# Kernel tuning notes

Hardware: AMD Instinct MI355X
Metric: run time of the kernel (lower is better)

The kernel has to match this reference:

```python
import jax, jax.numpy as jnp
import numpy as np

# irreps: 16x0e + 8x1o ; sh: 1x0e + 1x1o
M0, M1 = 16, 8
N_NODES, N_EDGES, N_BASIS = 10000, 160000, 8
DIM = M0 + 3 * M1                      # 40
NW = M0*M0 + M0*M1 + M1*M1 + M1*M0     # 576 per-edge TP weights
LOG2 = 0.6931471805599453


def _split(x):
    return x[:, :M0], x[:, M0:].reshape(-1, M1, 3)


def _merge(xs, xv):
    return jnp.concatenate([xs, xv.reshape(xv.shape[0], -1)], axis=1)


def _lin(x, Ws, Wv):
    # e3nn o3.Linear: per-irrep channel mixing, 1/sqrt(fan_in) path norm
    xs, xv = _split(x)
    return _merge(xs @ Ws / np.sqrt(M0),
                  jnp.einsum('nui,uv->nvi', xv, Wv) / np.sqrt(M1))


def _ssp(x):  # ShiftedSoftPlus
    return jax.nn.softplus(x) - LOG2


def setup_inputs() -> dict:
    key = jax.random.key(0)
    k = jax.random.split(key, 14)
    return {
        'x': jax.random.normal(k[0], (N_NODES, DIM), jnp.float32),
        'edge_radial': jax.random.uniform(k[1], (N_EDGES, N_BASIS), dtype=jnp.float32),
        'edge_sh': jax.random.normal(k[2], (N_EDGES, 4), jnp.float32),
        'edge_src': jax.random.randint(k[3], (N_EDGES,), 0, N_NODES),
        'edge_dst': jax.random.randint(k[4], (N_EDGES,), 0, N_NODES),
        'n_nodes': N_NODES,
        'W1s': jax.random.normal(k[5], (M0, M0), jnp.float32),
        'W1v': jax.random.normal(k[6], (M1, M1), jnp.float32),
        'Wfc': jax.random.normal(k[7], (N_BASIS, NW), jnp.float32),
        'W2s': jax.random.normal(k[8], (M0, M0), jnp.float32),
        'W2v': jax.random.normal(k[9], (M1, M1), jnp.float32),
        'R00': jax.random.normal(k[10], (M0, M0, M0), jnp.float32),
        'R01': jax.random.normal(k[11], (M0, M1, M1), jnp.float32),
        'R10': jax.random.normal(k[12], (M1, M0, M1), jnp.float32),
        'R11': jax.random.normal(k[13], (M1, M1, M0), jnp.float32),
    }


def reference(x, edge_radial, edge_sh, edge_src, edge_dst, n_nodes,
              W1s, W1v, Wfc, W2s, W2v, R00, R01, R10, R11):
    inv2 = 1.0 / np.sqrt(2.0)

    # linear_1
    h = _lin(x, W1s, W1v)
    hs, hv = _split(h)

    # SO3Convolution: per-edge TP weights from radial net
    sh0, sh1 = edge_sh[:, 0], edge_sh[:, 1:4]
    w = edge_radial @ Wfc / np.sqrt(N_BASIS)  # [E, NW]
    o = 0
    w00 = w[:, o:o + M0*M0].reshape(-1, M0, M0); o += M0*M0  # 0e x 0e -> 0e
    w01 = w[:, o:o + M0*M1].reshape(-1, M0, M1); o += M0*M1  # 0e x 1o -> 1o
    w10 = w[:, o:o + M1*M1].reshape(-1, M1, M1); o += M1*M1  # 1o x 0e -> 1o
    w11 = w[:, o:o + M1*M0].reshape(-1, M1, M0)              # 1o x 1o -> 0e (CG: delta/sqrt(3))

    xs_e, xv_e = hs[edge_src], hv[edge_src]  # gather
    msg_s = (jnp.einsum('eu,e,euw->ew', xs_e, sh0, w00) / np.sqrt(M0)
             + jnp.einsum('eui,ei,euw->ew', xv_e, sh1, w11) / np.sqrt(3.0 * M1)) * inv2
    msg_v = (jnp.einsum('eu,ei,euw->ewi', xs_e, sh1, w01) / np.sqrt(M0)
             + jnp.einsum('eui,e,euw->ewi', xv_e, sh0, w10) / np.sqrt(M1)) * inv2

    deg = np.sqrt(N_EDGES / N_NODES)
    outs = jax.ops.segment_sum(msg_s, edge_dst, num_segments=n_nodes) / deg
    outv = jax.ops.segment_sum(msg_v, edge_dst, num_segments=n_nodes) / deg

    # linear_2
    h = _lin(_merge(outs, outv), W2s, W2v)
    hs, hv = _split(h)

    # NormActivation (normalize=True, ShiftedSoftPlus, eps=1e-8)
    eps = 1e-8
    ns = jnp.sqrt(hs * hs + eps * eps)
    hs = hs / ns * _ssp(ns)
    nv = jnp.sqrt(jnp.sum(hv * hv, -1, keepdims=True) + eps * eps)
    hv = hv / nv * _ssp(nv)
    out = _merge(hs, hv)

    # residual FullyConnectedTensorProduct(x, x)
    xs, xv = _split(x)
    rs = (jnp.einsum('nu,nv,uvw->nw', xs, xs, R00) / M0
          + jnp.einsum('nui,nvi,uvw->nw', xv, xv, R11) / np.sqrt(3.0 * M1 * M1)) * inv2
    rv = (jnp.einsum('nu,nvi,uvw->nwi', xs, xv, R01) / np.sqrt(M0 * M1)
          + jnp.einsum('nui,nv,uvw->nwi', xv, xs, R10) / np.sqrt(M1 * M0)) * inv2

    return out + _merge(rs, rv)
```

## Files before the change

kernel.cpp:

```cpp
#include <hip/hip_runtime.h>
#include <math.h>

constexpr int kM0 = 16, kM1 = 8, kDim = 40, kNW = 576;
constexpr int kNodes = 10000, kEdges = 160000;
constexpr int kCap = 96;
constexpr int kNB = 24;

__device__ __forceinline__ float sspf(float x){
  float ax = fabsf(x);
  return fmaxf(x, 0.f) + log1pf(expf(-ax)) - 0.69314718055994531f;
}

__global__ void __launch_bounds__(256) k_pre(
    const float* __restrict__ x, const float* __restrict__ W1s,
    const float* __restrict__ W1v, const float* __restrict__ Wfc,
    const int* __restrict__ edst,
    float* __restrict__ h, float* __restrict__ WfcT,
    int* __restrict__ cnt, int* __restrict__ posw){
  int t = blockIdx.x*256 + threadIdx.x;
  posw[t] = atomicAdd(&cnt[edst[t]], 1);
  if (t < kNW){
    #pragma unroll
    for (int b=0;b<8;++b) WfcT[t*8+b] = Wfc[b*kNW + t];
  }
  if (t < kNodes){
    const float4* xp4 = (const float4*)(x + (size_t)t*kDim);
    float xx[40];
    #pragma unroll
    for (int i=0;i<10;++i){
      float4 v = xp4[i];
      xx[i*4]=v.x; xx[i*4+1]=v.y; xx[i*4+2]=v.z; xx[i*4+3]=v.w;
    }
    float hh[40];
    #pragma unroll
    for (int v=0; v<kM0; ++v){
      float acc = 0.f;
      #pragma unroll
      for (int u=0; u<kM0; ++u) acc += xx[u]*W1s[u*kM0+v];
      hh[v] = acc*0.25f;
    }
    #pragma unroll
    for (int v=0; v<kM1; ++v){
      float a0=0.f,a1=0.f,a2=0.f;
      #pragma unroll
      for (int u=0; u<kM1; ++u){
        float wv = W1v[u*kM1+v];
        a0 += xx[16+u*3+0]*wv;
        a1 += xx[16+u*3+1]*wv;
        a2 += xx[16+u*3+2]*wv;
      }
      hh[16+v*3+0]=a0*0.35355339059327373f;
      hh[16+v*3+1]=a1*0.35355339059327373f;
      hh[16+v*3+2]=a2*0.35355339059327373f;
    }
    float4* hp4 = (float4*)(h + (size_t)t*kDim);
    #pragma unroll
    for (int i=0;i<10;++i)
      hp4[i] = make_float4(hh[i*4],hh[i*4+1],hh[i*4+2],hh[i*4+3]);
  }
}

__global__ void __launch_bounds__(512) k_edge(
    const float* __restrict__ er, const float* __restrict__ esh,
    const int* __restrict__ esrc, const int* __restrict__ edst,
    const int* __restrict__ posw,
    const float* __restrict__ h, const float* __restrict__ WfcT,
    float* __restrict__ msg){
  __shared__ float sh_h[64][41];
  int t = threadIdx.x;
  int e0 = blockIdx.x*64;
  for (int idx = t; idx < 640; idx += 512){
    int el = idx/10, c4 = idx - el*10;
    int src = esrc[e0 + el];
    const float4 v = *(const float4*)(h + (size_t)src*kDim + c4*4);
    float* d = &sh_h[el][c4*4];
    d[0]=v.x; d[1]=v.y; d[2]=v.z; d[3]=v.w;
  }
  __syncthreads();

  int lane = t & 63;
  int q = __builtin_amdgcn_readfirstlane(t >> 6);
  int e = e0 + lane;
  float4 ra = *(const float4*)(er + (size_t)e*8);
  float4 rb = *(const float4*)(er + (size_t)e*8 + 4);
  const float r0=ra.x,r1=ra.y,r2=ra.z,r3=ra.w,r4=rb.x,r5=rb.y,r6=rb.z,r7=rb.w;
  float4 s4 = *(const float4*)(esh + (size_t)e*4);
  const float* hl = sh_h[lane];
  float* mp = msg + ((size_t)edst[e]*kCap + posw[e])*kDim;

#define DOT8(p) ((p)[0]*r0+(p)[1]*r1+(p)[2]*r2+(p)[3]*r3+(p)[4]*r4+(p)[5]*r5+(p)[6]*r6+(p)[7]*r7)

  const int w0 = q*2;
  float t00a=0.f, t00b=0.f, t11a=0.f, t11b=0.f;
  float t01=0.f, tx=0.f, ty=0.f, tz=0.f;

  #pragma unroll
  for (int u=0;u<16;++u){
    float xu = hl[u];
    const float* p0 = WfcT + (size_t)(u*16 + w0)*8;
    t00a += xu*DOT8(p0);
    t00b += xu*DOT8(p0 + 8);
    const float* p1 = WfcT + (size_t)(256 + u*8 + q)*8;
    t01 += xu*DOT8(p1);
  }
  #pragma unroll
  for (int u=0;u<8;++u){
    float v0=hl[16+u*3], v1=hl[16+u*3+1], v2=hl[16+u*3+2];
    float au = v0*s4.y + v1*s4.z + v2*s4.w;
    const float* p3 = WfcT + (size_t)(448 + u*16 + w0)*8;
    t11a += au*DOT8(p3);
    t11b += au*DOT8(p3 + 8);
    const float* p2 = WfcT + (size_t)(384 + u*8 + q)*8;
    float a = DOT8(p2);
    tx += v0*a; ty += v1*a; tz += v2*a;
  }
#undef DOT8

  constexpr float cs00 = 0.0625f;
  constexpr float cs11 = 0.05103103630798288f;
  constexpr float cv01 = 0.0625f;
  constexpr float cv10 = 0.08838834764831845f;

  *(float2*)(mp + w0) = make_float2(s4.x*t00a*cs00 + t11a*cs11,
                                    s4.x*t00b*cs00 + t11b*cs11);
  float va = t01*cv01, sc0 = s4.x*cv10;
  float* vp = mp + 16 + q*3;
  vp[0] = s4.y*va + tx*sc0;
  vp[1] = s4.z*va + ty*sc0;
  vp[2] = s4.w*va + tz*sc0;
}

__global__ void __launch_bounds__(960) k_node(
    const float* __restrict__ x, const float* __restrict__ msg,
    const int* __restrict__ cnt,
    const float* __restrict__ W2s, const float* __restrict__ W2v,
    const float* __restrict__ R00, const float* __restrict__ R01,
    const float* __restrict__ R10, const float* __restrict__ R11,
    float* __restrict__ out){
  __shared__ float sR00[4096], sR01[1024], sR10[1024], sR11[1024];
  __shared__ float sW2s[256], sW2v[64];
  __shared__ float sx[kNB][40], sa[kNB][40];
  __shared__ float4 sred[kNB][4][10];
  int t = threadIdx.x;
  for (int i=t; i<1024; i+=960) ((float4*)sR00)[i] = ((const float4*)R00)[i];
  if (t < 256){
    ((float4*)sR01)[t] = ((const float4*)R01)[t];
    ((float4*)sR10)[t] = ((const float4*)R10)[t];
    ((float4*)sR11)[t] = ((const float4*)R11)[t];
  }
  if (t >= 256 && t < 320) ((float4*)sW2s)[t-256] = ((const float4*)W2s)[t-256];
  if (t >= 320 && t < 336) ((float4*)sW2v)[t-320] = ((const float4*)W2v)[t-320];
  int nb = blockIdx.x*kNB;
  {
    int ns = t/40; int rem = t - ns*40; int kq = rem/10; int c4 = rem - kq*10;
    int n = nb + ns;
    float4 acc = make_float4(0.f,0.f,0.f,0.f);
    if (n < kNodes){
      int deg = cnt[n];
      const float* bp = msg + (size_t)n*kCap*kDim + c4*4;
      for (int k=kq; k<deg; k+=4){
        const float4 v = *(const float4*)(bp + (size_t)k*kDim);
        acc.x+=v.x; acc.y+=v.y; acc.z+=v.z; acc.w+=v.w;
      }
    }
    sred[ns][kq][c4] = acc;
  }
  __syncthreads();
  if (t < kNB*10){
    int ns = t/10, c4 = t - ns*10, n = nb+ns;
    float4 a0 = sred[ns][0][c4], a1 = sred[ns][1][c4];
    float4 a2 = sred[ns][2][c4], a3 = sred[ns][3][c4];
    sa[ns][c4*4+0] = (a0.x+a1.x+a2.x+a3.x)*0.25f;
    sa[ns][c4*4+1] = (a0.y+a1.y+a2.y+a3.y)*0.25f;
    sa[ns][c4*4+2] = (a0.z+a1.z+a2.z+a3.z)*0.25f;
    sa[ns][c4*4+3] = (a0.w+a1.w+a2.w+a3.w)*0.25f;
    float4 xv = (n < kNodes) ? *(const float4*)(x + (size_t)n*kDim + c4*4)
                             : make_float4(0.f,0.f,0.f,0.f);
    sx[ns][c4*4+0]=xv.x; sx[ns][c4*4+1]=xv.y; sx[ns][c4*4+2]=xv.z; sx[ns][c4*4+3]=xv.w;
  }
  __syncthreads();
  if (t < kNB*16){
    int ns = t>>4, w = t&15, n = nb+ns;
    const float* ap = sa[ns];
    const float* xp = sx[ns];
    float hsum = 0.f;
    #pragma unroll
    for (int u=0;u<16;++u) hsum += ap[u]*sW2s[u*16+w];
    hsum *= 0.25f;
    float nrm = sqrtf(hsum*hsum + 1e-16f);
    float val = hsum/nrm*sspf(nrm);
    float xs[16];
    #pragma unroll
    for (int v=0;v<16;++v) xs[v] = xp[v];
    float r0 = 0.f;
    #pragma unroll
    for (int u=0;u<16;++u){
      float tacc = 0.f;
      #pragma unroll
      for (int v=0;v<16;++v) tacc += xs[v]*sR00[(u*16+v)*16+w];
      r0 += xs[u]*tacc;
    }
    float xv[24];
    #pragma unroll
    for (int c2=0;c2<24;++c2) xv[c2] = xp[16+c2];
    float r1 = 0.f;
    #pragma unroll
    for (int u=0;u<8;++u){
      #pragma unroll
      for (int v=0;v<8;++v){
        float dot = xv[u*3]*xv[v*3] + xv[u*3+1]*xv[v*3+1] + xv[u*3+2]*xv[v*3+2];
        r1 += dot*sR11[(u*8+v)*16+w];
      }
    }
    if (n < kNodes)
      out[(size_t)n*kDim + w] = val + 0.04419417382415922f*r0 + 0.05103103630798288f*r1;
  } else if (t >= kNB*16 && t < kNB*16 + kNB*24) {
    int t2 = t - kNB*16;
    int ns = t2/24, cc = t2 - ns*24, w = cc/3, i = cc - w*3, n = nb+ns;
    const float* ap = sa[ns] + 16;
    const float* xp = sx[ns];
    float h0=0.f,h1=0.f,h2=0.f;
    #pragma unroll
    for (int u=0;u<8;++u){
      float wv = sW2v[u*8+w];
      h0 += ap[u*3+0]*wv; h1 += ap[u*3+1]*wv; h2 += ap[u*3+2]*wv;
    }
    const float sc = 0.35355339059327373f;
    h0*=sc; h1*=sc; h2*=sc;
    float nv = sqrtf(h0*h0+h1*h1+h2*h2 + 1e-16f);
    float hi = (i==0)?h0:((i==1)?h1:h2);
    float val = hi/nv*sspf(nv);
    float xs[16];
    #pragma unroll
    for (int v=0;v<16;++v) xs[v] = xp[v];
    float xvi[8];
    #pragma unroll
    for (int v=0;v<8;++v) xvi[v] = xp[16+v*3+i];
    float racc = 0.f;
    #pragma unroll
    for (int u=0;u<16;++u){
      float tacc=0.f;
      #pragma unroll
      for (int v=0;v<8;++v) tacc += xvi[v]*sR01[(u*8+v)*8+w];
      racc += xs[u]*tacc;
    }
    #pragma unroll
    for (int u=0;u<8;++u){
      float tacc=0.f;
      #pragma unroll
      for (int v=0;v<16;++v) tacc += xs[v]*sR10[(u*16+v)*8+w];
      racc += xvi[u]*tacc;
    }
    if (n < kNodes)
      out[(size_t)n*kDim + 16 + cc] = val + 0.0625f*racc;
  }
}

extern "C" void kernel_launch(void* const* d_in, const int* in_sizes, int n_in,
                              void* d_out, int out_size, void* d_ws, size_t ws_size,
                              hipStream_t stream){
  const float* x   = (const float*)d_in[0];
  const float* er  = (const float*)d_in[1];
  const float* esh = (const float*)d_in[2];
  const int*   esrc= (const int*)d_in[3];
  const int*   edst= (const int*)d_in[4];
  const float* W1s = (const float*)d_in[6];
  const float* W1v = (const float*)d_in[7];
  const float* Wfc = (const float*)d_in[8];
  const float* W2s = (const float*)d_in[9];
  const float* W2v = (const float*)d_in[10];
  const float* R00 = (const float*)d_in[11];
  const float* R01 = (const float*)d_in[12];
  const float* R10 = (const float*)d_in[13];
  const float* R11 = (const float*)d_in[14];
  float* out = (float*)d_out;

  char* wsb = (char*)d_ws;
  float* h    = (float*)wsb;
  float* msg  = h + (size_t)kNodes*kDim;
  float* WfcT = msg + (size_t)kNodes*kCap*kDim;
  int*   cnt  = (int*)(WfcT + (size_t)kNW*8);
  int*   posw = cnt + kNodes;

  hipMemsetAsync(cnt, 0, kNodes*sizeof(int), stream);
  k_pre<<<kEdges/256, 256, 0, stream>>>(x, W1s, W1v, Wfc, edst, h, WfcT, cnt, posw);
  k_edge<<<kEdges/64, 512, 0, stream>>>(er, esh, esrc, edst, posw, h, WfcT, msg);
  k_node<<<(kNodes+kNB-1)/kNB, 960, 0, stream>>>(x, msg, cnt, W2s, W2v, R00, R01, R10, R11, out);
}
```

Measured before the change: 155.1 us.

## Fuse linear_1 and destination slot assignment into edge kernel, drop memset

Moves the per-node linear_1 into the edge kernel: each block gathers raw x rows for its 64 source nodes into shared memory and applies W1s/W1v there, so the intermediate h buffer is no longer written and read. The per-edge atomic slot assignment also moves into the edge kernel, which removes the posw array. The memset of the counters becomes a tiny setup kernel that also transposes Wfc. The cost is that linear_1 is recomputed once per edge instead of once per node (16x redundant), and there is an extra barrier plus more shared memory per block.

```diff
diff --git a/kernel.cpp b/kernel.cpp
--- a/kernel.cpp
+++ b/kernel.cpp
@@ -11,82 +11,75 @@
   return fmaxf(x, 0.f) + log1pf(expf(-ax)) - 0.69314718055994531f;
 }
 
-__global__ void __launch_bounds__(256) k_pre(
-    const float* __restrict__ x, const float* __restrict__ W1s,
-    const float* __restrict__ W1v, const float* __restrict__ Wfc,
-    const int* __restrict__ edst,
-    float* __restrict__ h, float* __restrict__ WfcT,
-    int* __restrict__ cnt, int* __restrict__ posw){
-  int t = blockIdx.x*256 + threadIdx.x;
-  posw[t] = atomicAdd(&cnt[edst[t]], 1);
+__global__ void __launch_bounds__(1024) k_setup(
+    const float* __restrict__ Wfc, float* __restrict__ WfcT, int* __restrict__ cnt){
+  int t = blockIdx.x*1024 + threadIdx.x;
+  if (t < kNodes) cnt[t] = 0;
   if (t < kNW){
     #pragma unroll
     for (int b=0;b<8;++b) WfcT[t*8+b] = Wfc[b*kNW + t];
-  }
-  if (t < kNodes){
-    const float4* xp4 = (const float4*)(x + (size_t)t*kDim);
-    float xx[40];
-    #pragma unroll
-    for (int i=0;i<10;++i){
-      float4 v = xp4[i];
-      xx[i*4]=v.x; xx[i*4+1]=v.y; xx[i*4+2]=v.z; xx[i*4+3]=v.w;
-    }
-    float hh[40];
-    #pragma unroll
-    for (int v=0; v<kM0; ++v){
-      float acc = 0.f;
-      #pragma unroll
-      for (int u=0; u<kM0; ++u) acc += xx[u]*W1s[u*kM0+v];
-      hh[v] = acc*0.25f;
-    }
-    #pragma unroll
-    for (int v=0; v<kM1; ++v){
-      float a0=0.f,a1=0.f,a2=0.f;
-      #pragma unroll
-      for (int u=0; u<kM1; ++u){
-        float wv = W1v[u*kM1+v];
-        a0 += xx[16+u*3+0]*wv;
-        a1 += xx[16+u*3+1]*wv;
-        a2 += xx[16+u*3+2]*wv;
-      }
-      hh[16+v*3+0]=a0*0.35355339059327373f;
-      hh[16+v*3+1]=a1*0.35355339059327373f;
-      hh[16+v*3+2]=a2*0.35355339059327373f;
-    }
-    float4* hp4 = (float4*)(h + (size_t)t*kDim);
-    #pragma unroll
-    for (int i=0;i<10;++i)
-      hp4[i] = make_float4(hh[i*4],hh[i*4+1],hh[i*4+2],hh[i*4+3]);
   }
 }
 
 __global__ void __launch_bounds__(512) k_edge(
     const float* __restrict__ er, const float* __restrict__ esh,
     const int* __restrict__ esrc, const int* __restrict__ edst,
-    const int* __restrict__ posw,
-    const float* __restrict__ h, const float* __restrict__ WfcT,
-    float* __restrict__ msg){
+    const float* __restrict__ x, const float* __restrict__ W1s,
+    const float* __restrict__ W1v, const float* __restrict__ WfcT,
+    float* __restrict__ msg, int* __restrict__ cnt){
+  __shared__ float sh_x[64][41];
   __shared__ float sh_h[64][41];
+  __shared__ int   smp[64];
   int t = threadIdx.x;
+  int lane = t & 63;
+  int q = __builtin_amdgcn_readfirstlane(t >> 6);
   int e0 = blockIdx.x*64;
+
+  int myoff = 0;
+  if (q == 0){
+    int dst = edst[e0 + lane];
+    int pos = atomicAdd(&cnt[dst], 1);
+    myoff = (dst*kCap + pos)*kDim;
+  }
   for (int idx = t; idx < 640; idx += 512){
     int el = idx/10, c4 = idx - el*10;
     int src = esrc[e0 + el];
-    const float4 v = *(const float4*)(h + (size_t)src*kDim + c4*4);
-    float* d = &sh_h[el][c4*4];
+    const float4 v = *(const float4*)(x + (size_t)src*kDim + c4*4);
+    float* d = &sh_x[el][c4*4];
     d[0]=v.x; d[1]=v.y; d[2]=v.z; d[3]=v.w;
   }
-  __syncthreads();
-
-  int lane = t & 63;
-  int q = __builtin_amdgcn_readfirstlane(t >> 6);
+  if (q == 0) smp[lane] = myoff;
+  __syncthreads();
+
+  {
+    #pragma unroll
+    for (int k=0;k<5;++k){
+      const int c = q + 8*k;
+      float o;
+      if (c < 16){
+        float acc=0.f;
+        #pragma unroll
+        for (int u=0;u<16;++u) acc += sh_x[lane][u]*W1s[u*16+c];
+        o = acc*0.25f;
+      } else {
+        int j = c-16; int v = j/3, i = j-3*v;
+        float acc=0.f;
+        #pragma unroll
+        for (int u=0;u<8;++u) acc += sh_x[lane][16+u*3+i]*W1v[u*8+v];
+        o = acc*0.35355339059327373f;
+      }
+      sh_h[lane][c] = o;
+    }
+  }
+  __syncthreads();
+
   int e = e0 + lane;
   float4 ra = *(const float4*)(er + (size_t)e*8);
   float4 rb = *(const float4*)(er + (size_t)e*8 + 4);
   const float r0=ra.x,r1=ra.y,r2=ra.z,r3=ra.w,r4=rb.x,r5=rb.y,r6=rb.z,r7=rb.w;
   float4 s4 = *(const float4*)(esh + (size_t)e*4);
   const float* hl = sh_h[lane];
-  float* mp = msg + ((size_t)edst[e]*kCap + posw[e])*kDim;
+  float* mp = msg + smp[lane];
 
 #define DOT8(p) ((p)[0]*r0+(p)[1]*r1+(p)[2]*r2+(p)[3]*r3+(p)[4]*r4+(p)[5]*r5+(p)[6]*r6+(p)[7]*r7)
 
@@ -214,7 +207,7 @@
     }
     if (n < kNodes)
       out[(size_t)n*kDim + w] = val + 0.04419417382415922f*r0 + 0.05103103630798288f*r1;
-  } else if (t >= kNB*16 && t < kNB*16 + kNB*24) {
+  } else if (t < kNB*16 + kNB*24) {
     int t2 = t - kNB*16;
     int ns = t2/24, cc = t2 - ns*24, w = cc/3, i = cc - w*3, n = nb+ns;
     const float* ap = sa[ns] + 16;
@@ -276,14 +269,11 @@
   float* out = (float*)d_out;
 
   char* wsb = (char*)d_ws;
-  float* h    = (float*)wsb;
-  float* msg  = h + (size_t)kNodes*kDim;
+  float* msg  = (float*)wsb;
   float* WfcT = msg + (size_t)kNodes*kCap*kDim;
   int*   cnt  = (int*)(WfcT + (size_t)kNW*8);
-  int*   posw = cnt + kNodes;
-
-  hipMemsetAsync(cnt, 0, kNodes*sizeof(int), stream);
-  k_pre<<<kEdges/256, 256, 0, stream>>>(x, W1s, W1v, Wfc, edst, h, WfcT, cnt, posw);
-  k_edge<<<kEdges/64, 512, 0, stream>>>(er, esh, esrc, edst, posw, h, WfcT, msg);
+
+  k_setup<<<10, 1024, 0, stream>>>(Wfc, WfcT, cnt);
+  k_edge<<<kEdges/64, 512, 0, stream>>>(er, esh, esrc, edst, x, W1s, W1v, WfcT, msg, cnt);
   k_node<<<(kNodes+kNB-1)/kNB, 960, 0, stream>>>(x, msg, cnt, W2s, W2v, R00, R01, R10, R11, out);
 }
```

Measured after the change: 149.7 us. -3.5%, faster.
